# Kernel tuning notes

Measured on AMD Instinct MI355X. Metric: run time of the kernel, lower is better.

## Reference

```python
import jax, jax.numpy as jnp
import numpy as np


@jax.custom_vjp
def binarize(w):
    # Deterministic binarization: sign with ties (w==0) mapped to +1,
    # matching tf.where(w >= 0, 1.0, -1.0).
    return jnp.where(w >= 0, 1.0, -1.0).astype(w.dtype)


def _binarize_fwd(w):
    return binarize(w), w


def _binarize_bwd(w, g):
    # Straight-through estimator: pass grad where |w| < 1, else 0.
    return (jnp.where(jnp.abs(w) < 1.0, g, jnp.zeros_like(g)),)


binarize.defvjp(_binarize_fwd, _binarize_bwd)


def setup_inputs() -> dict:
    key = jax.random.key(0)
    kx, kw = jax.random.split(key)
    # NHWC activations
    x = jax.random.normal(kx, (32, 112, 112, 128), dtype=jnp.float32)
    # HWIO kernel (glorot-scale init so values straddle the +/- decision boundary)
    kernel = jax.random.normal(kw, (3, 3, 128, 256), dtype=jnp.float32) * 0.05
    return {"x": x, "kernel": kernel}


def reference(x, kernel):
    wb = binarize(kernel)  # [3,3,Cin,Cout] in {-1,+1}
    return jax.lax.conv_general_dilated(
        x, wb,
        window_strides=(1, 1),
        padding="SAME",
        dimension_numbers=("NHWC", "HWIO", "NHWC"),
    )
```

## Files before the change

### kernel.cpp

```cpp
#include <hip/hip_runtime.h>

typedef __attribute__((ext_vector_type(8))) short short8;
typedef __attribute__((ext_vector_type(4))) float f32x4;
typedef __attribute__((ext_vector_type(4))) unsigned short u16x4;
typedef __attribute__((ext_vector_type(8))) unsigned short u16x8;

#define H 112
#define W 112
#define HP 114
#define WP 114
#define CIN 128
#define COUT 256
#define NPIX (H * W)
#define NIMG 32
#define MTOT (NIMG * NPIX)
#define PADELEMS ((long)NIMG * HP * WP * CIN)

__device__ __forceinline__ unsigned short f2bf(float f) {
    unsigned int u = __builtin_bit_cast(unsigned int, f);
    u += 0x7FFFu + ((u >> 16) & 1u);
    return (unsigned short)(u >> 16);
}

__device__ __forceinline__ void gl2lds16(const void* g, void* l) {
    __builtin_amdgcn_global_load_lds(
        (const __attribute__((address_space(1))) unsigned int*)g,
        (__attribute__((address_space(3))) unsigned int*)l,
        16, 0, 0);
}

__global__ void binw_kernel(const float* __restrict__ kw, unsigned short* __restrict__ bw) {
    int tid = blockIdx.x * 256 + threadIdx.x;
    int cin5 = tid & 31;
    int cout = (tid >> 5) & 255;
    int kc4  = (tid >> 13) & 3;
    int tap  = tid >> 15;
    int cin  = kc4 * 32 + cin5;
    float w = kw[(tap * 128 + cin) * 256 + cout];
    bw[tid] = (w >= 0.0f) ? (unsigned short)0x3F80u : (unsigned short)0xBF80u;
}

__global__ void pad_kernel(const float* __restrict__ x, unsigned short* __restrict__ xp) {
    long tid = (long)blockIdx.x * 256 + threadIdx.x;
    if (tid >= PADELEMS / 8) return;
    int c8 = (int)(tid & 15);
    long rem = tid >> 4;
    int wp = (int)(rem % WP); rem /= WP;
    int hp = (int)(rem % HP);
    int n  = (int)(rem / HP);
    u16x8 v = {0, 0, 0, 0, 0, 0, 0, 0};
    if (hp >= 1 && hp <= H && wp >= 1 && wp <= W) {
        const float* s = x + (((long)(n * H + hp - 1) * W + (wp - 1)) * CIN + c8 * 8);
        f32x4 a = *(const f32x4*)s;
        f32x4 b = *(const f32x4*)(s + 4);
        v = (u16x8){ f2bf(a.x), f2bf(a.y), f2bf(a.z), f2bf(a.w),
                     f2bf(b.x), f2bf(b.y), f2bf(b.z), f2bf(b.w) };
    }
    *(u16x8*)(xp + tid * 8) = v;
}

__global__ __launch_bounds__(256, 2)
void conv2_kernel(const unsigned short* __restrict__ xp, const unsigned short* __restrict__ bw,
                  float* __restrict__ out) {
    __shared__ unsigned short As[128 * 32];
    __shared__ unsigned short Bs[128 * 32];

    const int tid = threadIdx.x;
    const int bm = blockIdx.x;
    const int bn = blockIdx.y;
    const int lane = tid & 63;
    const int wv = tid >> 6;
    const int wr = wv >> 1, wc = wv & 1;

    long arowbase[2];
#pragma unroll
    for (int j = 0; j < 2; ++j) {
        int s = tid + j * 256;
        int p = bm * 128 + (s >> 2);
        int n = p / NPIX;
        int rem = p - n * NPIX;
        int oh = rem / W, ow = rem - oh * W;
        arowbase[j] = (long)((n * HP + oh + 1) * WP + (ow + 1)) * CIN + (s & 3) * 8;
    }

    f32x4 acc[4][4];
#pragma unroll
    for (int m = 0; m < 4; ++m)
#pragma unroll
        for (int n = 0; n < 4; ++n)
            acc[m][n] = (f32x4){0.f, 0.f, 0.f, 0.f};

    const int arow = wr * 64 + (lane & 15);
    const int brow = wc * 64 + (lane & 15);
    const int koff = (lane >> 4) * 8;

    for (int t = 0; t < 36; ++t) {
        const int tap = t >> 2, kc = t & 3;
        const int dh = tap / 3 - 1, dw = tap % 3 - 1;
        const long shift = (long)(dh * WP + dw) * CIN + kc * 32;

#pragma unroll
        for (int j = 0; j < 2; ++j)
            gl2lds16(xp + arowbase[j] + shift, &As[(j * 256 + wv * 64) * 8]);
#pragma unroll
        for (int j = 0; j < 2; ++j)
            gl2lds16(bw + (tap * 4 + kc) * 8192 + bn * 4096 + (tid + j * 256) * 8,
                     &Bs[(j * 256 + wv * 64) * 8]);

        __syncthreads();

        short8 af[4], bfr[4];
#pragma unroll
        for (int m = 0; m < 4; ++m)
            af[m] = *(const short8*)&As[(arow + m * 16) * 32 + koff];
#pragma unroll
        for (int n = 0; n < 4; ++n)
            bfr[n] = *(const short8*)&Bs[(brow + n * 16) * 32 + koff];
#pragma unroll
        for (int m = 0; m < 4; ++m)
#pragma unroll
            for (int n = 0; n < 4; ++n)
                acc[m][n] = __builtin_amdgcn_mfma_f32_16x16x32_bf16(af[m], bfr[n], acc[m][n], 0, 0, 0);

        __syncthreads();
    }

    const long row0 = (long)bm * 128 + wr * 64 + ((lane >> 4) * 4);
    const int col = bn * 128 + wc * 64 + (lane & 15);
#pragma unroll
    for (int m = 0; m < 4; ++m)
#pragma unroll
        for (int n = 0; n < 4; ++n)
#pragma unroll
            for (int j = 0; j < 4; ++j)
                out[(row0 + m * 16 + j) * COUT + col + n * 16] = acc[m][n][j];
}

__global__ __launch_bounds__(256, 2)
void conv_fallback_kernel(const float* __restrict__ x, const unsigned short* __restrict__ bw,
                          float* __restrict__ out) {
    __shared__ unsigned short As[128][40];
    __shared__ unsigned short Bs[128][40];
    const int tid = threadIdx.x;
    const int bm = blockIdx.x, bn = blockIdx.y;
    const int lane = tid & 63;
    const int wv = tid >> 6;
    const int wr = wv >> 1, wc = wv & 1;
    const int c4 = (tid & 7) * 4;
    const int rseg = tid >> 3;
    int ohs[4], ows[4], bases[4];
#pragma unroll
    for (int i = 0; i < 4; ++i) {
        int p = bm * 128 + rseg + i * 32;
        int n = p / NPIX;
        int rem = p - n * NPIX;
        int oh = rem / W, ow = rem - oh * W;
        ohs[i] = oh; ows[i] = ow;
        bases[i] = ((n * H + oh) * W + ow) * CIN;
    }
    f32x4 acc[4][4];
#pragma unroll
    for (int m = 0; m < 4; ++m)
#pragma unroll
        for (int n = 0; n < 4; ++n)
            acc[m][n] = (f32x4){0.f, 0.f, 0.f, 0.f};
    const int arow = wr * 64 + (lane & 15);
    const int brow = wc * 64 + (lane & 15);
    const int koff = (lane >> 4) * 8;
    for (int tap = 0; tap < 9; ++tap) {
        const int dh = tap / 3 - 1, dw = tap % 3 - 1;
        const int shift = (dh * W + dw) * CIN;
#pragma unroll
        for (int kc = 0; kc < 4; ++kc) {
            __syncthreads();
#pragma unroll
            for (int i = 0; i < 4; ++i) {
                int ih = ohs[i] + dh, iw = ows[i] + dw;
                bool valid = ((unsigned)ih < (unsigned)H) & ((unsigned)iw < (unsigned)W);
                f32x4 v = {0.f, 0.f, 0.f, 0.f};
                if (valid) v = *(const f32x4*)(x + bases[i] + shift + kc * 32 + c4);
                u16x4 s = { f2bf(v.x), f2bf(v.y), f2bf(v.z), f2bf(v.w) };
                *(u16x4*)&As[rseg + i * 32][c4] = s;
            }
            const unsigned short* bp = bw + tap * 32768 + kc * 8192 + bn * 4096;
#pragma unroll
            for (int j = 0; j < 2; ++j) {
                int idx = tid + j * 256;
                *(u16x8*)&Bs[idx >> 2][(idx & 3) * 8] = *(const u16x8*)(bp + (idx >> 2) * 32 + (idx & 3) * 8);
            }
            __syncthreads();
            short8 af[4], bfr[4];
#pragma unroll
            for (int m = 0; m < 4; ++m)
                af[m] = *(const short8*)&As[arow + m * 16][koff];
#pragma unroll
            for (int n = 0; n < 4; ++n)
                bfr[n] = *(const short8*)&Bs[brow + n * 16][koff];
#pragma unroll
            for (int m = 0; m < 4; ++m)
#pragma unroll
                for (int n = 0; n < 4; ++n)
                    acc[m][n] = __builtin_amdgcn_mfma_f32_16x16x32_bf16(af[m], bfr[n], acc[m][n], 0, 0, 0);
        }
    }
    const long row0 = (long)bm * 128 + wr * 64 + ((lane >> 4) * 4);
    const int col = bn * 128 + wc * 64 + (lane & 15);
#pragma unroll
    for (int m = 0; m < 4; ++m)
#pragma unroll
        for (int n = 0; n < 4; ++n)
#pragma unroll
            for (int j = 0; j < 4; ++j)
                out[(row0 + m * 16 + j) * COUT + col + n * 16] = acc[m][n][j];
}

extern "C" void kernel_launch(void* const* d_in, const int* in_sizes, int n_in,
                              void* d_out, int out_size, void* d_ws, size_t ws_size,
                              hipStream_t stream) {
    const float* x  = (const float*)d_in[0];
    const float* kw = (const float*)d_in[1];
    float* out = (float*)d_out;
    unsigned short* bw = (unsigned short*)d_ws;
    const size_t BW_BYTES = 9 * 4 * 256 * 32 * 2;
    const size_t PAD_BYTES = (size_t)PADELEMS * 2;

    binw_kernel<<<(9 * 256 * 128) / 256, 256, 0, stream>>>(kw, bw);

    if (ws_size >= BW_BYTES + PAD_BYTES) {
        unsigned short* xp = (unsigned short*)((char*)d_ws + BW_BYTES);
        pad_kernel<<<(int)((PADELEMS / 8 + 255) / 256), 256, 0, stream>>>(x, xp);
        dim3 grid(MTOT / 128, COUT / 128);
        conv2_kernel<<<grid, 256, 0, stream>>>(xp, bw, out);
    } else {
        dim3 grid(MTOT / 128, COUT / 128);
        conv_fallback_kernel<<<grid, 256, 0, stream>>>(x, bw, out);
    }
}
```

Before: 363.6 us.

## Stage padded input halo once per K-chunk and reuse across all nine taps

Replaces the per-tap implicit-GEMM loop with a 512-thread, 512-pixel tile. Each 32-channel chunk stages the halo of padded input rows into LDS once, and all nine 3x3 taps read from it at shifted offsets. Binarized weights are re-laid out and streamed straight from global memory into double-buffered registers instead of LDS. A block-index swizzle is added for locality. This cuts redundant global-to-LDS traffic and barriers, at the cost of a larger LDS footprint, more accumulator registers, and possible LDS bank conflicts from the shifted reads.

```diff
diff --git a/kernel.cpp b/kernel.cpp
--- a/kernel.cpp
+++ b/kernel.cpp
@@ -15,6 +15,7 @@
 #define NIMG 32
 #define MTOT (NIMG * NPIX)
 #define PADELEMS ((long)NIMG * HP * WP * CIN)
+#define NPADPIX (NIMG * HP * WP)
 
 __device__ __forceinline__ unsigned short f2bf(float f) {
     unsigned int u = __builtin_bit_cast(unsigned int, f);
@@ -29,13 +30,21 @@
         16, 0, 0);
 }
 
-__global__ void binw_kernel(const float* __restrict__ kw, unsigned short* __restrict__ bw) {
+__device__ __forceinline__ int pidx(int p) {
+    int n = p / NPIX;
+    int r = p - n * NPIX;
+    int oh = r / W, ow = r - oh * W;
+    return n * (HP * WP) + (oh + 1) * WP + ow + 1;
+}
+
+__global__ void binw3_kernel(const float* __restrict__ kw, unsigned short* __restrict__ bw) {
     int tid = blockIdx.x * 256 + threadIdx.x;
-    int cin5 = tid & 31;
-    int cout = (tid >> 5) & 255;
-    int kc4  = (tid >> 13) & 3;
+    int e    = tid & 7;
+    int cout = (tid >> 3) & 255;
+    int q    = (tid >> 11) & 3;
+    int kc   = (tid >> 13) & 3;
     int tap  = tid >> 15;
-    int cin  = kc4 * 32 + cin5;
+    int cin  = kc * 32 + q * 8 + e;
     float w = kw[(tap * 128 + cin) * 256 + cout];
     bw[tid] = (w >= 0.0f) ? (unsigned short)0x3F80u : (unsigned short)0xBF80u;
 }
@@ -59,81 +68,109 @@
     *(u16x8*)(xp + tid * 8) = v;
 }
 
-__global__ __launch_bounds__(256, 2)
-void conv2_kernel(const unsigned short* __restrict__ xp, const unsigned short* __restrict__ bw,
+__global__ __launch_bounds__(512, 2)
+void conv9_kernel(const unsigned short* __restrict__ xp, const unsigned short* __restrict__ bw,
                   float* __restrict__ out) {
-    __shared__ unsigned short As[128 * 32];
-    __shared__ unsigned short Bs[128 * 32];
+    __shared__ unsigned short Ah[4 * 1024 * 8];
 
     const int tid = threadIdx.x;
-    const int bm = blockIdx.x;
-    const int bn = blockIdx.y;
+    const int swz = (blockIdx.x & 7) * 196 + (blockIdx.x >> 3);
+    const int bm = swz >> 1;
+    const int bn = swz & 1;
     const int lane = tid & 63;
     const int wv = tid >> 6;
-    const int wr = wv >> 1, wc = wv & 1;
-
-    long arowbase[2];
-#pragma unroll
-    for (int j = 0; j < 2; ++j) {
-        int s = tid + j * 256;
-        int p = bm * 128 + (s >> 2);
-        int n = p / NPIX;
-        int rem = p - n * NPIX;
-        int oh = rem / W, ow = rem - oh * W;
-        arowbase[j] = (long)((n * HP + oh + 1) * WP + (ow + 1)) * CIN + (s & 3) * 8;
-    }
-
-    f32x4 acc[4][4];
-#pragma unroll
-    for (int m = 0; m < 4; ++m)
+    const int wr = wv >> 1;
+    const int wc = wv & 1;
+    const int l15 = lane & 15;
+
+    const int pfirst = bm * 512;
+    const int h0 = pidx(pfirst) - 115;
+
+    int al[8];
+#pragma unroll
+    for (int m = 0; m < 8; ++m) {
+        int p = pfirst + wr * 128 + m * 16 + l15;
+        al[m] = ((lane >> 4) << 14) + (pidx(p) - h0 - 115) * 16;
+    }
+    const unsigned short* bbase = bw + ((lane >> 4) * 256 + bn * 128 + wc * 64 + l15) * 8;
+
+#define HSTAGE(KC) do {                                                         \
+        _Pragma("unroll")                                                       \
+        for (int j = 0; j < 8; ++j) {                                           \
+            int s = j * 512 + tid;                                              \
+            int kq = s >> 10, q = s & 1023;                                     \
+            if (h0 + q < NPADPIX)                                               \
+                gl2lds16(xp + (long)(h0 + q) * CIN + (KC) * 32 + kq * 8,        \
+                         &Ah[(kq * 1024 + q) * 8]);                             \
+        }                                                                       \
+    } while (0)
+
+    f32x4 acc[8][4];
+#pragma unroll
+    for (int m = 0; m < 8; ++m)
 #pragma unroll
         for (int n = 0; n < 4; ++n)
             acc[m][n] = (f32x4){0.f, 0.f, 0.f, 0.f};
 
-    const int arow = wr * 64 + (lane & 15);
-    const int brow = wc * 64 + (lane & 15);
-    const int koff = (lane >> 4) * 8;
-
-    for (int t = 0; t < 36; ++t) {
-        const int tap = t >> 2, kc = t & 3;
+    short8 breg[2][4];
+#pragma unroll
+    for (int n = 0; n < 4; ++n)
+        breg[0][n] = *(const short8*)(bbase + n * 128);
+
+    const char* ah = (const char*)&Ah[0];
+
+#pragma unroll
+    for (int st = 0; st < 36; ++st) {
+        const int kc = st / 9, tap = st % 9;
+        if (tap == 0) {
+            __syncthreads();
+            HSTAGE(kc);
+            __syncthreads();
+        }
+        if (st < 35) {
+            const int st2 = st + 1, kc2 = st2 / 9, tap2 = st2 % 9;
+#pragma unroll
+            for (int n = 0; n < 4; ++n)
+                breg[st2 & 1][n] = *(const short8*)(bbase + (tap2 * 4 + kc2) * 8192 + n * 128);
+        }
         const int dh = tap / 3 - 1, dw = tap % 3 - 1;
-        const long shift = (long)(dh * WP + dw) * CIN + kc * 32;
-
-#pragma unroll
-        for (int j = 0; j < 2; ++j)
-            gl2lds16(xp + arowbase[j] + shift, &As[(j * 256 + wv * 64) * 8]);
-#pragma unroll
-        for (int j = 0; j < 2; ++j)
-            gl2lds16(bw + (tap * 4 + kc) * 8192 + bn * 4096 + (tid + j * 256) * 8,
-                     &Bs[(j * 256 + wv * 64) * 8]);
-
-        __syncthreads();
-
-        short8 af[4], bfr[4];
-#pragma unroll
-        for (int m = 0; m < 4; ++m)
-            af[m] = *(const short8*)&As[(arow + m * 16) * 32 + koff];
-#pragma unroll
-        for (int n = 0; n < 4; ++n)
-            bfr[n] = *(const short8*)&Bs[(brow + n * 16) * 32 + koff];
-#pragma unroll
-        for (int m = 0; m < 4; ++m)
-#pragma unroll
-            for (int n = 0; n < 4; ++n)
-                acc[m][n] = __builtin_amdgcn_mfma_f32_16x16x32_bf16(af[m], bfr[n], acc[m][n], 0, 0, 0);
-
-        __syncthreads();
-    }
-
-    const long row0 = (long)bm * 128 + wr * 64 + ((lane >> 4) * 4);
-    const int col = bn * 128 + wc * 64 + (lane & 15);
-#pragma unroll
-    for (int m = 0; m < 4; ++m)
+        const int tshb = (dh * WP + dw + 115) * 16;
+#pragma unroll
+        for (int mh = 0; mh < 2; ++mh) {
+            short8 afr[4];
+#pragma unroll
+            for (int mi = 0; mi < 4; ++mi)
+                afr[mi] = *(const short8*)(ah + al[mh * 4 + mi] + tshb);
+#pragma unroll
+            for (int mi = 0; mi < 4; ++mi)
+#pragma unroll
+                for (int n = 0; n < 4; ++n)
+                    acc[mh * 4 + mi][n] = __builtin_amdgcn_mfma_f32_16x16x32_bf16(
+                        afr[mi], breg[st & 1][n], acc[mh * 4 + mi][n], 0, 0, 0);
+        }
+    }
+#undef HSTAGE
+
+    const long row0 = (long)pfirst + wr * 128 + (lane >> 4) * 4;
+    const int col = bn * 128 + wc * 64 + l15;
+#pragma unroll
+    for (int m = 0; m < 8; ++m)
 #pragma unroll
         for (int n = 0; n < 4; ++n)
 #pragma unroll
             for (int j = 0; j < 4; ++j)
                 out[(row0 + m * 16 + j) * COUT + col + n * 16] = acc[m][n][j];
+}
+
+__global__ void binw_kernel(const float* __restrict__ kw, unsigned short* __restrict__ bw) {
+    int tid = blockIdx.x * 256 + threadIdx.x;
+    int cin5 = tid & 31;
+    int cout = (tid >> 5) & 255;
+    int kc4  = (tid >> 13) & 3;
+    int tap  = tid >> 15;
+    int cin  = kc4 * 32 + cin5;
+    float w = kw[(tap * 128 + cin) * 256 + cout];
+    bw[tid] = (w >= 0.0f) ? (unsigned short)0x3F80u : (unsigned short)0xBF80u;
 }
 
 __global__ __launch_bounds__(256, 2)
@@ -221,17 +258,16 @@
     const float* kw = (const float*)d_in[1];
     float* out = (float*)d_out;
     unsigned short* bw = (unsigned short*)d_ws;
-    const size_t BW_BYTES = 9 * 4 * 256 * 32 * 2;
+    const size_t BW_BYTES = 9 * 4 * 4 * 256 * 8 * 2;
     const size_t PAD_BYTES = (size_t)PADELEMS * 2;
 
-    binw_kernel<<<(9 * 256 * 128) / 256, 256, 0, stream>>>(kw, bw);
-
     if (ws_size >= BW_BYTES + PAD_BYTES) {
+        binw3_kernel<<<(9 * 4 * 4 * 256 * 8) / 256, 256, 0, stream>>>(kw, bw);
         unsigned short* xp = (unsigned short*)((char*)d_ws + BW_BYTES);
         pad_kernel<<<(int)((PADELEMS / 8 + 255) / 256), 256, 0, stream>>>(x, xp);
-        dim3 grid(MTOT / 128, COUT / 128);
-        conv2_kernel<<<grid, 256, 0, stream>>>(xp, bw, out);
+        conv9_kernel<<<(MTOT / 512) * 2, 512, 0, stream>>>(xp, bw, out);
     } else {
+        binw_kernel<<<(9 * 256 * 128) / 256, 256, 0, stream>>>(kw, bw);
         dim3 grid(MTOT / 128, COUT / 128);
         conv_fallback_kernel<<<grid, 256, 0, stream>>>(x, bw, out);
     }
```

New measurement: 435.2 us. +19.7%, slower.
